# Performance work log

Measured on AMD Instinct MI355X. Metric: run time of the kernel, lower is better.

Reference implementation:

```python
import jax, jax.numpy as jnp
import numpy as np

# Llama-2-7B-like GQA attention, prefill over packed equal-length sequences
H = 4096      # hidden_size
NH = 32       # num_attention_heads
NKV = 8       # num_key_value_heads
HD = H // NH  # head_dim = 128
B = 4         # number of packed sequences
S = 1024      # seq_len per sequence
T = B * S     # total packed tokens
BASE = 10000.0  # rope_theta


def setup_inputs() -> dict:
    key = jax.random.key(0)
    ks = jax.random.split(key, 5)
    x = jax.random.normal(ks[0], (T, H), jnp.float32)
    positions = jnp.tile(jnp.arange(S, dtype=jnp.int32), B)  # per-seq positions
    kv_cache = jnp.zeros((1,), jnp.float32)  # placeholder (prefill: kv from current tokens)
    init = 0.02
    wq = jax.random.normal(ks[1], (NH * HD, H), jnp.float32) * init
    wk = jax.random.normal(ks[2], (NKV * HD, H), jnp.float32) * init
    wv = jax.random.normal(ks[3], (NKV * HD, H), jnp.float32) * init
    wo = jax.random.normal(ks[4], (H, NH * HD), jnp.float32) * init
    return {"x": x, "positions": positions, "kv_cache": kv_cache,
            "wq": wq, "wk": wk, "wv": wv, "wo": wo, "seq_len": S}


def _rope(xh, cos_b, sin_b):
    # xh: [T, Hh, D]; cos_b/sin_b: [T, 1, D] (freqs repeat-interleaved by 2)
    half = xh.shape[-1] // 2
    x_rot = jnp.concatenate([-xh[..., half:], xh[..., :half]], axis=-1)
    return xh * cos_b + x_rot * sin_b


def reference(x, positions, kv_cache, wq, wk, wv, wo, seq_len):
    Tn = x.shape[0]
    q = (x @ wq.T).reshape(Tn, NH, HD)
    k = (x @ wk.T).reshape(Tn, NKV, HD)
    v = (x @ wv.T).reshape(Tn, NKV, HD)
    # GQA: repeat_interleave kv heads
    rep = NH // NKV
    k = jnp.repeat(k, rep, axis=1)
    v = jnp.repeat(v, rep, axis=1)
    # RoPE tables (faithful to _precompute_freqs/_rotary_embeddings)
    inv_freq = 1.0 / (BASE ** (jnp.arange(0, HD, 2, dtype=jnp.float32) / HD))
    t = jnp.arange(seq_len, dtype=jnp.float32)
    freqs = t[:, None] * inv_freq[None, :]            # [S, D/2]
    cos, sin = jnp.cos(freqs), jnp.sin(freqs)
    pos = jnp.clip(positions.astype(jnp.int32), 0, seq_len - 1)
    cos_b = jnp.repeat(cos[pos], 2, axis=-1)[:, None, :]  # [T,1,D]
    sin_b = jnp.repeat(sin[pos], 2, axis=-1)[:, None, :]
    q = _rope(q, cos_b, sin_b)
    k = _rope(k, cos_b, sin_b)
    # Paged attention (prefill): causal attention within each packed sequence
    Bn = Tn // seq_len
    qb = q.reshape(Bn, seq_len, NH, HD)
    kb = k.reshape(Bn, seq_len, NH, HD)
    vb = v.reshape(Bn, seq_len, NH, HD)
    scores = jnp.einsum('bqhd,bkhd->bhqk', qb, kb) * (HD ** -0.5)
    causal = jnp.tril(jnp.ones((seq_len, seq_len), bool))
    scores = jnp.where(causal[None, None], scores, -jnp.inf)
    probs = jax.nn.softmax(scores, axis=-1)
    out = jnp.einsum('bhqk,bkhd->bqhd', probs, vb).reshape(Tn, NH * HD)
    return out @ wo.T
```

## Files before the change

### kernel.cpp

```cpp
#include <hip/hip_runtime.h>
#include <hip/hip_bf16.h>
#include <math.h>

#define T_TOK 4096
#define HID   4096
#define NHQ   32
#define NKVH  8
#define HDIM  128
#define SEQ   1024
#define NBATCH 4

typedef __attribute__((ext_vector_type(8))) short bf16x8;
typedef __attribute__((ext_vector_type(4))) float f32x4;

__device__ __forceinline__ unsigned short f2bf(float f) {
  union { float f; unsigned int u; } x; x.f = f;
  unsigned int r = x.u + 0x7FFFu + ((x.u >> 16) & 1u);
  return (unsigned short)(r >> 16);
}

#define GLOAD_LDS16(gp, lp)                                                        \
  __builtin_amdgcn_global_load_lds(                                                \
      (__attribute__((address_space(1))) void*)(unsigned long long)(const void*)(gp), \
      (__attribute__((address_space(3))) void*)(unsigned long long)(const void*)(lp), \
      16, 0, 0)

__global__ __launch_bounds__(256) void cast_all_k(const float* __restrict__ x,
                                                  const float* __restrict__ wq,
                                                  const float* __restrict__ wk,
                                                  const float* __restrict__ wv,
                                                  const float* __restrict__ wo,
                                                  unsigned short* __restrict__ xb,
                                                  unsigned short* __restrict__ wqkv,
                                                  unsigned short* __restrict__ wob) {
  int i = blockIdx.x * 256 + threadIdx.x;
  const float* src; unsigned short* dst; int off;
  if (i < 4194304)       { src = x;  dst = xb;   off = i; }
  else if (i < 8388608)  { src = wq; dst = wqkv; off = i - 4194304; }
  else if (i < 9437184)  { src = wk; dst = wqkv + 16777216; off = i - 8388608; }
  else if (i < 10485760) { src = wv; dst = wqkv + 20971520; off = i - 9437184; }
  else                   { src = wo; dst = wob;  off = i - 10485760; }
  float4 f = ((const float4*)src)[off];
  ushort4 o;
  o.x = f2bf(f.x); o.y = f2bf(f.y); o.z = f2bf(f.z); o.w = f2bf(f.w);
  ((ushort4*)dst)[off] = o;
}

__global__ __launch_bounds__(512, 2) void gemm_qkv(const unsigned short* __restrict__ A,
                                                   const unsigned short* __restrict__ B,
                                                   const int* __restrict__ pos,
                                                   unsigned short* __restrict__ qr,
                                                   unsigned short* __restrict__ kr,
                                                   unsigned short* __restrict__ vbuf) {
  const int K = 4096, nt = 64;
  __shared__ unsigned short AS[3][16384];
  __shared__ unsigned short BS[3][8192];
  const int tid  = threadIdx.x;
  const int lane = tid & 63;
  const int wave = tid >> 6;
  const int m16  = lane & 15;
  const int quad = lane >> 4;
  const int wm   = wave >> 1;
  const int wn   = wave & 1;

  const int gx = 48;
  const int orig = blockIdx.y * gx + blockIdx.x;
  const int swz = (orig & 7) * 96 + (orig >> 3);
  const long rowBase = (long)(swz / gx) * 256;
  const long colBase = (long)(swz % gx) * 128;

  int aoff[2], boff[2];
#pragma unroll
  for (int ks = 0; ks < 2; ++ks) {
    int sx = ((ks * 4 + quad) ^ (m16 & 7)) * 8;
    aoff[ks] = (wm * 64 + m16) * 64 + sx;
    boff[ks] = (wn * 32 + m16) * 64 + sx;
  }

  const long Kl = K;
  const int sck = ((tid & 7) ^ ((tid >> 3) & 7)) * 8;
  const unsigned short* gA = A + (rowBase + (tid >> 3)) * Kl + sck;
  const unsigned short* gB = B + (colBase + (tid >> 3)) * Kl + sck;
  const int dofs = wave * 512;

#define STG_B(slot_, ko_) { GLOAD_LDS16(gB + (ko_),            &BS[slot_][dofs]);         \
                            GLOAD_LDS16(gB + (ko_) + 64 * Kl,  &BS[slot_][4096 + dofs]); }
#define STG_A(slot_, ko_) { GLOAD_LDS16(gA + (ko_),            &AS[slot_][dofs]);         \
                            GLOAD_LDS16(gA + (ko_) + 64 * Kl,  &AS[slot_][4096 + dofs]);  \
                            GLOAD_LDS16(gA + (ko_) + 128 * Kl, &AS[slot_][8192 + dofs]);  \
                            GLOAD_LDS16(gA + (ko_) + 192 * Kl, &AS[slot_][12288 + dofs]); }

  f32x4 acc[4][4] = {};

  STG_A(0, 0); STG_B(0, 0);
  STG_A(1, 64); STG_B(1, 64);
  asm volatile("s_waitcnt vmcnt(6)" ::: "memory");
  __builtin_amdgcn_s_barrier();

  for (int g = 0; g < 22; ++g) {
#pragma unroll
    for (int u = 0; u < 3; ++u) {
      const int t = g * 3 + u;
      if (t < nt) {
        const bool doStage = (t + 2) < nt;
        const long kn = (long)(t + 2) * 64;
        bf16x8 af[4][2], bfr[4][2];
#pragma unroll
        for (int mf = 0; mf < 4; ++mf)
          af[mf][0] = *(const bf16x8*)(&AS[u][aoff[0] + mf * 1024]);
#pragma unroll
        for (int nf = 0; nf < 4; ++nf)
          bfr[nf][0] = *(const bf16x8*)(&BS[u][boff[0] + (nf & 1) * 1024 + (nf >> 1) * 4096]);
        if (doStage) { STG_A((u + 2) % 3, kn); STG_B((u + 2) % 3, kn); }
#pragma unroll
        for (int mf = 0; mf < 4; ++mf)
          af[mf][1] = *(const bf16x8*)(&AS[u][aoff[1] + mf * 1024]);
#pragma unroll
        for (int nf = 0; nf < 4; ++nf)
          bfr[nf][1] = *(const bf16x8*)(&BS[u][boff[1] + (nf & 1) * 1024 + (nf >> 1) * 4096]);
        __builtin_amdgcn_s_setprio(1);
#pragma unroll
        for (int mf = 0; mf < 4; ++mf)
#pragma unroll
          for (int nf = 0; nf < 4; ++nf)
            acc[mf][nf] = __builtin_amdgcn_mfma_f32_16x16x32_bf16(af[mf][0], bfr[nf][0], acc[mf][nf], 0, 0, 0);
#pragma unroll
        for (int mf = 0; mf < 4; ++mf)
#pragma unroll
          for (int nf = 0; nf < 4; ++nf)
            acc[mf][nf] = __builtin_amdgcn_mfma_f32_16x16x32_bf16(af[mf][1], bfr[nf][1], acc[mf][nf], 0, 0, 0);
        __builtin_amdgcn_s_setprio(0);
        if (doStage)        asm volatile("s_waitcnt vmcnt(6)" ::: "memory");
        else if (t + 1 < nt) asm volatile("s_waitcnt vmcnt(0)" ::: "memory");
        __builtin_amdgcn_s_barrier();
      }
    }
  }

  const int n0 = (int)colBase;
  unsigned short* dst;
  int rstride, colofs;
  bool dorope;
  if (n0 < 4096)       { dst = qr;   rstride = NHQ * HDIM;  colofs = n0;        dorope = true; }
  else if (n0 < 5120)  { dst = kr;   rstride = NKVH * HDIM; colofs = n0 - 4096; dorope = true; }
  else                 { dst = vbuf; rstride = NKVH * HDIM; colofs = n0 - 5120; dorope = false; }
  const float c0 = -13.287712379549449f / 64.0f;
  float fA[2], fB[2];
#pragma unroll
  for (int e = 0; e < 2; ++e) {
    int d = wn * 32 + e * 16 + m16;
    fA[e] = exp2f(c0 * (float)(d >> 1));
    fB[e] = exp2f(c0 * (float)((d >> 1) + 32));
  }
#pragma unroll
  for (int mf = 0; mf < 4; ++mf) {
#pragma unroll
    for (int reg = 0; reg < 4; ++reg) {
      int grow = (int)rowBase + wm * 64 + mf * 16 + quad * 4 + reg;
      unsigned short* drow = dst + (long)grow * rstride + colofs;
      if (dorope) {
        int p = pos[grow];
        p = p < 0 ? 0 : (p > SEQ - 1 ? SEQ - 1 : p);
        float pf = (float)p;
#pragma unroll
        for (int e = 0; e < 2; ++e) {
          int d = wn * 32 + e * 16 + m16;
          float lo = acc[mf][e][reg], hi = acc[mf][e + 2][reg];
          float s1, cc1, s2, cc2;
          __sincosf(pf * fA[e], &s1, &cc1);
          __sincosf(pf * fB[e], &s2, &cc2);
          drow[d]      = f2bf(lo * cc1 - hi * s1);
          drow[d + 64] = f2bf(hi * cc2 + lo * s2);
        }
      } else {
#pragma unroll
        for (int e = 0; e < 2; ++e) {
          int d = wn * 32 + e * 16 + m16;
          drow[d]      = f2bf(acc[mf][e][reg]);
          drow[d + 64] = f2bf(acc[mf][e + 2][reg]);
        }
      }
    }
  }
}

__global__ __launch_bounds__(512, 2) void gemm_o(const unsigned short* __restrict__ A,
                                                 const unsigned short* __restrict__ B,
                                                 float* __restrict__ C) {
  const int K = 4096, N = 4096, nt = 128;
  __shared__ unsigned short AS[3][8192];
  __shared__ unsigned short BS[3][8192];
  const int tid  = threadIdx.x;
  const int lane = tid & 63;
  const int wave = tid >> 6;
  const int m16  = lane & 15;
  const int quad = lane >> 4;
  const int wm   = wave >> 2;
  const int wn   = wave & 3;

  const int gx = 16;
  const int orig = blockIdx.y * gx + blockIdx.x;
  const int swz = (orig & 7) * 32 + (orig >> 3);
  const long rowBase = (long)(swz / gx) * 256;
  const long colBase = (long)(swz % gx) * 256;

  const int slot8 = ((quad + 4 * (m16 & 1)) ^ (m16 >> 1)) * 8;
  const int aob = (wm * 64 + (m16 >> 1)) * 64 + slot8;
  const int bob = (wn * 32 + (m16 >> 1)) * 64 + slot8;

  const long Kl = K;
  const int z = (tid & 7) ^ ((tid >> 3) & 7);
  const long srow = 2 * (tid >> 3) + (z >> 2);
  const int sk = (z & 3) * 8;
  const unsigned short* oA = A + (rowBase + srow) * Kl + sk;
  const unsigned short* oB = B + (colBase + srow) * Kl + sk;
  const int dofs = wave * 512;

#define OSTG_A(sl_, ko_) { GLOAD_LDS16(oA + (ko_),            &AS[sl_][dofs]);         \
                           GLOAD_LDS16(oA + (ko_) + 128 * Kl, &AS[sl_][4096 + dofs]); }
#define OSTG_B(sl_, ko_) { GLOAD_LDS16(oB + (ko_),            &BS[sl_][dofs]);         \
                           GLOAD_LDS16(oB + (ko_) + 128 * Kl, &BS[sl_][4096 + dofs]); }

  f32x4 acc[8][4] = {};

  OSTG_A(0, 0);  OSTG_B(0, 0);
  OSTG_A(1, 32); OSTG_B(1, 32);
  asm volatile("s_waitcnt vmcnt(4)" ::: "memory");
  __builtin_amdgcn_s_barrier();

  for (int g = 0; g < 43; ++g) {
#pragma unroll
    for (int u = 0; u < 3; ++u) {
      const int t = g * 3 + u;
      if (t < nt) {
        const bool doStage = (t + 2) < nt;
        const long kn = (long)(t + 2) * 32;
        bf16x8 af[8], bfr[4];
#pragma unroll
        for (int nf = 0; nf < 4; ++nf)
          bfr[nf] = *(const bf16x8*)(&BS[u][bob + nf * 512]);
#pragma unroll
        for (int mf = 0; mf < 4; ++mf)
          af[mf] = *(const bf16x8*)(&AS[u][aob + mf * 512]);
        if (doStage) { OSTG_A((u + 2) % 3, kn); OSTG_B((u + 2) % 3, kn); }
#pragma unroll
        for (int mf = 4; mf < 8; ++mf)
          af[mf] = *(const bf16x8*)(&AS[u][aob + mf * 512]);
        __builtin_amdgcn_s_setprio(1);
#pragma unroll
        for (int mf = 0; mf < 4; ++mf)
#pragma unroll
          for (int nf = 0; nf < 4; ++nf)
            acc[mf][nf] = __builtin_amdgcn_mfma_f32_16x16x32_bf16(af[mf], bfr[nf], acc[mf][nf], 0, 0, 0);
#pragma unroll
        for (int mf = 4; mf < 8; ++mf)
#pragma unroll
          for (int nf = 0; nf < 4; ++nf)
            acc[mf][nf] = __builtin_amdgcn_mfma_f32_16x16x32_bf16(af[mf], bfr[nf], acc[mf][nf], 0, 0, 0);
        __builtin_amdgcn_s_setprio(0);
        if (doStage)         asm volatile("s_waitcnt vmcnt(4)" ::: "memory");
        else if (t + 1 < nt) asm volatile("s_waitcnt vmcnt(0)" ::: "memory");
        __builtin_amdgcn_s_barrier();
      }
    }
  }

#pragma unroll
  for (int mf = 0; mf < 8; ++mf)
#pragma unroll
    for (int nf = 0; nf < 4; ++nf) {
      long c = colBase + wn * 64 + nf * 16 + m16;
#pragma unroll
      for (int reg = 0; reg < 4; ++reg) {
        long row = rowBase + wm * 128 + mf * 16 + quad * 4 + reg;
        C[row * N + c] = acc[mf][nf][reg];
      }
    }
}

#define ATT_SCALE_L2 0.12754227022f
__global__ __launch_bounds__(256) void attn_k(const unsigned short* __restrict__ Qp,
                                              const unsigned short* __restrict__ Kp,
                                              const unsigned short* __restrict__ Vp,
                                              unsigned short* __restrict__ Op) {
  const int pr = blockIdx.x, h = blockIdx.y, b = blockIdx.z;
  const int kvh = h >> 2;
  const int tid = threadIdx.x, wave = tid >> 6, lane = tid & 63;
  const int m16 = lane & 15, quad = lane >> 4;

  __shared__ unsigned short Ks[2][64][128];
  __shared__ unsigned short Vt[2][128][64];
  __shared__ unsigned short Ps[4][32][64];

  const unsigned short* Kh = Kp + (long)(b * SEQ) * (NKVH * HDIM) + kvh * HDIM;
  const unsigned short* Vh = Vp + (long)(b * SEQ) * (NKVH * HDIM) + kvh * HDIM;

#define STAGE_K(ktv, bufp) {                                               \
    _Pragma("unroll")                                                      \
    for (int it_ = 0; it_ < 4; ++it_) {                                    \
      int c_ = it_ * 256 + tid;                                            \
      int row_ = c_ >> 4, psg_ = c_ & 15;                                  \
      int sg_ = (psg_ & 8) | ((psg_ & 7) ^ (row_ & 7));                    \
      GLOAD_LDS16(Kh + ((long)(ktv) * 64 + row_) * (NKVH * HDIM) + sg_ * 8,\
                  ((unsigned short*)(bufp)) + (it_ * 256 + wave * 64) * 8);\
    } }

#define LOAD_V(ktv, dvv) {                                                 \
    _Pragma("unroll")                                                      \
    for (int it_ = 0; it_ < 4; ++it_)                                      \
      dvv[it_] = *(const uint4*)(Vh + ((long)(ktv) * 64 + lane) * (NKVH * HDIM) + (it_ * 4 + wave) * 8); }

#define SCATTER_V(bufp, dvv) {                                             \
    _Pragma("unroll")                                                      \
    for (int it_ = 0; it_ < 4; ++it_) {                                    \
      const unsigned short* pv_ = (const unsigned short*)&dvv[it_];        \
      int seg_ = it_ * 4 + wave;                                           \
      _Pragma("unroll")                                                    \
      for (int e_ = 0; e_ < 8; ++e_) {                                     \
        int d_ = seg_ * 8 + e_;                                            \
        (bufp)[d_][((((lane >> 3) + d_) & 7) * 8) + (lane & 7)] = pv_[e_]; \
      } } }

  for (int pass = 0; pass < 2; ++pass) {
    const int qt = pass ? pr : (7 - pr);
    const int qbase = qt * 128;
    const int wq_lo = qbase + wave * 32;

    bf16x8 qa[2][4];
#pragma unroll
    for (int i = 0; i < 2; ++i) {
      const unsigned short* qrow =
          Qp + (long)(b * SEQ + wq_lo + i * 16 + m16) * (NHQ * HDIM) + h * HDIM;
#pragma unroll
      for (int kk = 0; kk < 4; ++kk)
        qa[i][kk] = *(const bf16x8*)(qrow + kk * 32 + quad * 8);
    }

    f32x4 o[2][8] = {};
    float mrow[2][4], lrow[2][4];
#pragma unroll
    for (int i = 0; i < 2; ++i)
#pragma unroll
      for (int r = 0; r < 4; ++r) { mrow[i][r] = -1e30f; lrow[i][r] = 0.f; }

    const int nkt = qt * 2 + 2;

    {
      STAGE_K(0, Ks[0]);
      uint4 dv[4];
      LOAD_V(0, dv);
      asm volatile("s_waitcnt vmcnt(0)" ::: "memory");
      SCATTER_V(Vt[0], dv);
    }
    __syncthreads();

    for (int kt = 0; kt < nkt; ++kt) {
      const int cb = kt & 1;
      const bool active = (kt * 64) <= (wq_lo + 31);
      const bool more = (kt + 1) < nkt;

      f32x4 s4[2][4] = {};
      if (active) {
        __builtin_amdgcn_s_setprio(1);
#pragma unroll
        for (int kk = 0; kk < 4; ++kk) {
          bf16x8 kbf[4];
#pragma unroll
          for (int j = 0; j < 4; ++j) {
            int row = j * 16 + m16;
            int cl = kk * 4 + quad;
            int ps = (cl & 8) | ((cl & 7) ^ (row & 7));
            kbf[j] = *(const bf16x8*)(&Ks[cb][row][ps * 8]);
          }
#pragma unroll
          for (int i = 0; i < 2; ++i)
#pragma unroll
            for (int j = 0; j < 4; ++j)
              s4[i][j] = __builtin_amdgcn_mfma_f32_16x16x32_bf16(qa[i][kk], kbf[j], s4[i][j], 0, 0, 0);
        }
        __builtin_amdgcn_s_setprio(0);
      }

      uint4 dv[4];
      if (more) {
        STAGE_K(kt + 1, Ks[cb ^ 1]);
        LOAD_V(kt + 1, dv);
      }
      asm volatile("" ::: "memory");

      if (active) {
        const bool full = (kt * 64 + 63) <= wq_lo;
#pragma unroll
        for (int i = 0; i < 2; ++i) {
#pragma unroll
          for (int r = 0; r < 4; ++r) {
            const int qrow = i * 16 + quad * 4 + r;
            const int qi = qbase + wave * 32 + qrow;
            float v[4];
#pragma unroll
            for (int j = 0; j < 4; ++j) {
              v[j] = s4[i][j][r] * ATT_SCALE_L2;
              if (!full && (kt * 64 + j * 16 + m16 > qi)) v[j] = -1e30f;
            }
            float mx = fmaxf(fmaxf(v[0], v[1]), fmaxf(v[2], v[3]));
            mx = fmaxf(mx, __shfl_xor(mx, 1));
            mx = fmaxf(mx, __shfl_xor(mx, 2));
            mx = fmaxf(mx, __shfl_xor(mx, 4));
            mx = fmaxf(mx, __shfl_xor(mx, 8));
            float mold = mrow[i][r];
            float mnew = fmaxf(mold, mx);
            float alpha = exp2f(mold - mnew);
            float rs = 0.f;
#pragma unroll
            for (int j = 0; j < 4; ++j) {
              float pj = exp2f(v[j] - mnew);
              rs += pj;
              int col = j * 16 + m16;
              Ps[wave][qrow][((((col >> 3) + qrow) & 7) * 8) + (col & 7)] = f2bf(pj);
            }
            rs += __shfl_xor(rs, 1); rs += __shfl_xor(rs, 2);
            rs += __shfl_xor(rs, 4); rs += __shfl_xor(rs, 8);
            lrow[i][r] = lrow[i][r] * alpha + rs;
            mrow[i][r] = mnew;
#pragma unroll
            for (int n = 0; n < 8; ++n) o[i][n][r] *= alpha;
          }
        }
        __builtin_amdgcn_s_setprio(1);
#pragma unroll
        for (int kk = 0; kk < 2; ++kk) {
          bf16x8 pa[2], vb[8];
#pragma unroll
          for (int i = 0; i < 2; ++i) {
            int row = i * 16 + m16;
            pa[i] = *(const bf16x8*)(&Ps[wave][row][(((kk * 4 + quad) + row) & 7) * 8]);
          }
#pragma unroll
          for (int n = 0; n < 8; ++n) {
            int row = n * 16 + m16;
            vb[n] = *(const bf16x8*)(&Vt[cb][row][(((kk * 4 + quad) + row) & 7) * 8]);
          }
#pragma unroll
          for (int i = 0; i < 2; ++i)
#pragma unroll
            for (int n = 0; n < 8; ++n)
              o[i][n] = __builtin_amdgcn_mfma_f32_16x16x32_bf16(pa[i], vb[n], o[i][n], 0, 0, 0);
        }
        __builtin_amdgcn_s_setprio(0);
      }

      if (more) {
        asm volatile("s_waitcnt vmcnt(0)" ::: "memory");
        SCATTER_V(Vt[cb ^ 1], dv);
      }
      __syncthreads();
    }

#pragma unroll
    for (int i = 0; i < 2; ++i) {
#pragma unroll
      for (int r = 0; r < 4; ++r) {
        float inv = 1.0f / lrow[i][r];
        unsigned short* orow =
            Op + (long)(b * SEQ + wq_lo + i * 16 + quad * 4 + r) * (NHQ * HDIM) + h * HDIM;
#pragma unroll
        for (int n = 0; n < 8; ++n)
          orow[n * 16 + m16] = f2bf(o[i][n][r] * inv);
      }
    }
  }
}

extern "C" void kernel_launch(void* const* d_in, const int* in_sizes, int n_in,
                              void* d_out, int out_size, void* d_ws, size_t ws_size,
                              hipStream_t stream) {
  (void)in_sizes; (void)n_in; (void)out_size; (void)ws_size;
  const float* x  = (const float*)d_in[0];
  const int* pos  = (const int*)d_in[1];
  const float* wq = (const float*)d_in[3];
  const float* wk = (const float*)d_in[4];
  const float* wv = (const float*)d_in[5];
  const float* wo = (const float*)d_in[6];
  float* out = (float*)d_out;

  char* ws = (char*)d_ws;
  unsigned short* xb    = (unsigned short*)(ws);
  unsigned short* wqkv  = (unsigned short*)(ws + (32ll << 20));
  unsigned short* wob   = (unsigned short*)(ws + (80ll << 20));
  unsigned short* qr    = (unsigned short*)(ws + (112ll << 20));
  unsigned short* kr    = (unsigned short*)(ws + (144ll << 20));
  unsigned short* vb_   = (unsigned short*)(ws + (152ll << 20));
  unsigned short* ao    = (unsigned short*)(ws + (160ll << 20));

  cast_all_k<<<57344, 256, 0, stream>>>(x, wq, wk, wv, wo, xb, wqkv, wob);
  gemm_qkv<<<dim3(48, 16), 512, 0, stream>>>(xb, wqkv, pos, qr, kr, vb_);
  attn_k<<<dim3(4, 32, 4), 256, 0, stream>>>(qr, kr, vb_, ao);
  gemm_o<<<dim3(16, 16), 512, 0, stream>>>(ao, wob, out);
}
```

Baseline: 744.4 us.

## Split GEMM k-step into two barrier-synchronized half phases to interleave loads and MFMA

Both the QKV-projection GEMM and the output-projection GEMM inner loops are restructured into two sub-phases per k-tile. Each phase loads a half set of fragments from LDS, issues part of the next-tile global-to-LDS staging (A in one phase, B in the other), then synchronizes with a barrier and waits on LDS counters before running that half's MFMAs. This is a ping-pong style schedule meant to keep waves in lockstep, halve fragment register pressure, and spread global loads across the step. It adds two extra barriers per iteration, which may cost time if the waves were already overlapping well.

```diff
diff --git a/kernel.cpp b/kernel.cpp
--- a/kernel.cpp
+++ b/kernel.cpp
@@ -104,33 +104,43 @@
       if (t < nt) {
         const bool doStage = (t + 2) < nt;
         const long kn = (long)(t + 2) * 64;
-        bf16x8 af[4][2], bfr[4][2];
-#pragma unroll
-        for (int mf = 0; mf < 4; ++mf)
-          af[mf][0] = *(const bf16x8*)(&AS[u][aoff[0] + mf * 1024]);
+        bf16x8 af[4], bfr[4];
+
+#pragma unroll
+        for (int mf = 0; mf < 4; ++mf)
+          af[mf] = *(const bf16x8*)(&AS[u][aoff[0] + mf * 1024]);
 #pragma unroll
         for (int nf = 0; nf < 4; ++nf)
-          bfr[nf][0] = *(const bf16x8*)(&BS[u][boff[0] + (nf & 1) * 1024 + (nf >> 1) * 4096]);
-        if (doStage) { STG_A((u + 2) % 3, kn); STG_B((u + 2) % 3, kn); }
-#pragma unroll
-        for (int mf = 0; mf < 4; ++mf)
-          af[mf][1] = *(const bf16x8*)(&AS[u][aoff[1] + mf * 1024]);
+          bfr[nf] = *(const bf16x8*)(&BS[u][boff[0] + (nf & 1) * 1024 + (nf >> 1) * 4096]);
+        if (doStage) STG_A((u + 2) % 3, kn);
+        __builtin_amdgcn_s_barrier();
+        asm volatile("s_waitcnt lgkmcnt(0)" ::: "memory");
+        __builtin_amdgcn_s_setprio(1);
+#pragma unroll
+        for (int mf = 0; mf < 4; ++mf)
+#pragma unroll
+          for (int nf = 0; nf < 4; ++nf)
+            acc[mf][nf] = __builtin_amdgcn_mfma_f32_16x16x32_bf16(af[mf], bfr[nf], acc[mf][nf], 0, 0, 0);
+        __builtin_amdgcn_s_setprio(0);
+        __builtin_amdgcn_s_barrier();
+
+#pragma unroll
+        for (int mf = 0; mf < 4; ++mf)
+          af[mf] = *(const bf16x8*)(&AS[u][aoff[1] + mf * 1024]);
 #pragma unroll
         for (int nf = 0; nf < 4; ++nf)
-          bfr[nf][1] = *(const bf16x8*)(&BS[u][boff[1] + (nf & 1) * 1024 + (nf >> 1) * 4096]);
+          bfr[nf] = *(const bf16x8*)(&BS[u][boff[1] + (nf & 1) * 1024 + (nf >> 1) * 4096]);
+        if (doStage) STG_B((u + 2) % 3, kn);
+        __builtin_amdgcn_s_barrier();
+        asm volatile("s_waitcnt lgkmcnt(0)" ::: "memory");
         __builtin_amdgcn_s_setprio(1);
 #pragma unroll
         for (int mf = 0; mf < 4; ++mf)
 #pragma unroll
           for (int nf = 0; nf < 4; ++nf)
-            acc[mf][nf] = __builtin_amdgcn_mfma_f32_16x16x32_bf16(af[mf][0], bfr[nf][0], acc[mf][nf], 0, 0, 0);
-#pragma unroll
-        for (int mf = 0; mf < 4; ++mf)
-#pragma unroll
-          for (int nf = 0; nf < 4; ++nf)
-            acc[mf][nf] = __builtin_amdgcn_mfma_f32_16x16x32_bf16(af[mf][1], bfr[nf][1], acc[mf][nf], 0, 0, 0);
+            acc[mf][nf] = __builtin_amdgcn_mfma_f32_16x16x32_bf16(af[mf], bfr[nf], acc[mf][nf], 0, 0, 0);
         __builtin_amdgcn_s_setprio(0);
-        if (doStage)        asm volatile("s_waitcnt vmcnt(6)" ::: "memory");
+        if (doStage)         asm volatile("s_waitcnt vmcnt(6)" ::: "memory");
         else if (t + 1 < nt) asm volatile("s_waitcnt vmcnt(0)" ::: "memory");
         __builtin_amdgcn_s_barrier();
       }
@@ -235,28 +245,38 @@
       if (t < nt) {
         const bool doStage = (t + 2) < nt;
         const long kn = (long)(t + 2) * 32;
-        bf16x8 af[8], bfr[4];
+        bf16x8 af[4], bfr[4];
+
 #pragma unroll
         for (int nf = 0; nf < 4; ++nf)
           bfr[nf] = *(const bf16x8*)(&BS[u][bob + nf * 512]);
 #pragma unroll
         for (int mf = 0; mf < 4; ++mf)
           af[mf] = *(const bf16x8*)(&AS[u][aob + mf * 512]);
-        if (doStage) { OSTG_A((u + 2) % 3, kn); OSTG_B((u + 2) % 3, kn); }
-#pragma unroll
-        for (int mf = 4; mf < 8; ++mf)
-          af[mf] = *(const bf16x8*)(&AS[u][aob + mf * 512]);
+        if (doStage) OSTG_A((u + 2) % 3, kn);
+        __builtin_amdgcn_s_barrier();
+        asm volatile("s_waitcnt lgkmcnt(0)" ::: "memory");
         __builtin_amdgcn_s_setprio(1);
 #pragma unroll
         for (int mf = 0; mf < 4; ++mf)
 #pragma unroll
           for (int nf = 0; nf < 4; ++nf)
             acc[mf][nf] = __builtin_amdgcn_mfma_f32_16x16x32_bf16(af[mf], bfr[nf], acc[mf][nf], 0, 0, 0);
-#pragma unroll
-        for (int mf = 4; mf < 8; ++mf)
+        __builtin_amdgcn_s_setprio(0);
+        __builtin_amdgcn_s_barrier();
+
+#pragma unroll
+        for (int mf = 0; mf < 4; ++mf)
+          af[mf] = *(const bf16x8*)(&AS[u][aob + (4 + mf) * 512]);
+        if (doStage) OSTG_B((u + 2) % 3, kn);
+        __builtin_amdgcn_s_barrier();
+        asm volatile("s_waitcnt lgkmcnt(0)" ::: "memory");
+        __builtin_amdgcn_s_setprio(1);
+#pragma unroll
+        for (int mf = 0; mf < 4; ++mf)
 #pragma unroll
           for (int nf = 0; nf < 4; ++nf)
-            acc[mf][nf] = __builtin_amdgcn_mfma_f32_16x16x32_bf16(af[mf], bfr[nf], acc[mf][nf], 0, 0, 0);
+            acc[4 + mf][nf] = __builtin_amdgcn_mfma_f32_16x16x32_bf16(af[mf], bfr[nf], acc[4 + mf][nf], 0, 0, 0);
         __builtin_amdgcn_s_setprio(0);
         if (doStage)         asm volatile("s_waitcnt vmcnt(4)" ::: "memory");
         else if (t + 1 < nt) asm volatile("s_waitcnt vmcnt(0)" ::: "memory");
```

New measurement: 750.0 us. About the same (+0.8%).

## Unify QKV and output GEMMs into one 256x256-tile kernel with 4-stage pipeline

Applied to the files above, without the earlier changes.

Replaces the separate QKV GEMM (256x128 tiles, 3-stage) and output GEMM with a single templated 256x256-tile kernel. It uses a 4-slot LDS ring that prefetches three tiles ahead and reads the next tile's fragments from LDS right after the MFMAs, with the RoPE epilogue fused in for the QKV variant. The wave-to-column mapping changes so each wave's accumulator columns line up with RoPE head pairs. The attention kernel drops V double buffering in favour of a single Vt buffer plus an extra barrier. The aim is more data reuse and better load/compute overlap, at the cost of one block per CU (launch_bounds 512,1), fewer QKV blocks (384) and an added sync in attention.

```diff
diff --git a/kernel.cpp b/kernel.cpp
--- a/kernel.cpp
+++ b/kernel.cpp
@@ -46,150 +46,18 @@
   ((ushort4*)dst)[off] = o;
 }
 
-__global__ __launch_bounds__(512, 2) void gemm_qkv(const unsigned short* __restrict__ A,
-                                                   const unsigned short* __restrict__ B,
-                                                   const int* __restrict__ pos,
-                                                   unsigned short* __restrict__ qr,
-                                                   unsigned short* __restrict__ kr,
-                                                   unsigned short* __restrict__ vbuf) {
-  const int K = 4096, nt = 64;
-  __shared__ unsigned short AS[3][16384];
-  __shared__ unsigned short BS[3][8192];
-  const int tid  = threadIdx.x;
-  const int lane = tid & 63;
-  const int wave = tid >> 6;
-  const int m16  = lane & 15;
-  const int quad = lane >> 4;
-  const int wm   = wave >> 1;
-  const int wn   = wave & 1;
-
-  const int gx = 48;
-  const int orig = blockIdx.y * gx + blockIdx.x;
-  const int swz = (orig & 7) * 96 + (orig >> 3);
-  const long rowBase = (long)(swz / gx) * 256;
-  const long colBase = (long)(swz % gx) * 128;
-
-  int aoff[2], boff[2];
-#pragma unroll
-  for (int ks = 0; ks < 2; ++ks) {
-    int sx = ((ks * 4 + quad) ^ (m16 & 7)) * 8;
-    aoff[ks] = (wm * 64 + m16) * 64 + sx;
-    boff[ks] = (wn * 32 + m16) * 64 + sx;
-  }
-
-  const long Kl = K;
-  const int sck = ((tid & 7) ^ ((tid >> 3) & 7)) * 8;
-  const unsigned short* gA = A + (rowBase + (tid >> 3)) * Kl + sck;
-  const unsigned short* gB = B + (colBase + (tid >> 3)) * Kl + sck;
-  const int dofs = wave * 512;
-
-#define STG_B(slot_, ko_) { GLOAD_LDS16(gB + (ko_),            &BS[slot_][dofs]);         \
-                            GLOAD_LDS16(gB + (ko_) + 64 * Kl,  &BS[slot_][4096 + dofs]); }
-#define STG_A(slot_, ko_) { GLOAD_LDS16(gA + (ko_),            &AS[slot_][dofs]);         \
-                            GLOAD_LDS16(gA + (ko_) + 64 * Kl,  &AS[slot_][4096 + dofs]);  \
-                            GLOAD_LDS16(gA + (ko_) + 128 * Kl, &AS[slot_][8192 + dofs]);  \
-                            GLOAD_LDS16(gA + (ko_) + 192 * Kl, &AS[slot_][12288 + dofs]); }
-
-  f32x4 acc[4][4] = {};
-
-  STG_A(0, 0); STG_B(0, 0);
-  STG_A(1, 64); STG_B(1, 64);
-  asm volatile("s_waitcnt vmcnt(6)" ::: "memory");
-  __builtin_amdgcn_s_barrier();
-
-  for (int g = 0; g < 22; ++g) {
-#pragma unroll
-    for (int u = 0; u < 3; ++u) {
-      const int t = g * 3 + u;
-      if (t < nt) {
-        const bool doStage = (t + 2) < nt;
-        const long kn = (long)(t + 2) * 64;
-        bf16x8 af[4][2], bfr[4][2];
-#pragma unroll
-        for (int mf = 0; mf < 4; ++mf)
-          af[mf][0] = *(const bf16x8*)(&AS[u][aoff[0] + mf * 1024]);
-#pragma unroll
-        for (int nf = 0; nf < 4; ++nf)
-          bfr[nf][0] = *(const bf16x8*)(&BS[u][boff[0] + (nf & 1) * 1024 + (nf >> 1) * 4096]);
-        if (doStage) { STG_A((u + 2) % 3, kn); STG_B((u + 2) % 3, kn); }
-#pragma unroll
-        for (int mf = 0; mf < 4; ++mf)
-          af[mf][1] = *(const bf16x8*)(&AS[u][aoff[1] + mf * 1024]);
-#pragma unroll
-        for (int nf = 0; nf < 4; ++nf)
-          bfr[nf][1] = *(const bf16x8*)(&BS[u][boff[1] + (nf & 1) * 1024 + (nf >> 1) * 4096]);
-        __builtin_amdgcn_s_setprio(1);
-#pragma unroll
-        for (int mf = 0; mf < 4; ++mf)
-#pragma unroll
-          for (int nf = 0; nf < 4; ++nf)
-            acc[mf][nf] = __builtin_amdgcn_mfma_f32_16x16x32_bf16(af[mf][0], bfr[nf][0], acc[mf][nf], 0, 0, 0);
-#pragma unroll
-        for (int mf = 0; mf < 4; ++mf)
-#pragma unroll
-          for (int nf = 0; nf < 4; ++nf)
-            acc[mf][nf] = __builtin_amdgcn_mfma_f32_16x16x32_bf16(af[mf][1], bfr[nf][1], acc[mf][nf], 0, 0, 0);
-        __builtin_amdgcn_s_setprio(0);
-        if (doStage)        asm volatile("s_waitcnt vmcnt(6)" ::: "memory");
-        else if (t + 1 < nt) asm volatile("s_waitcnt vmcnt(0)" ::: "memory");
-        __builtin_amdgcn_s_barrier();
-      }
-    }
-  }
-
-  const int n0 = (int)colBase;
-  unsigned short* dst;
-  int rstride, colofs;
-  bool dorope;
-  if (n0 < 4096)       { dst = qr;   rstride = NHQ * HDIM;  colofs = n0;        dorope = true; }
-  else if (n0 < 5120)  { dst = kr;   rstride = NKVH * HDIM; colofs = n0 - 4096; dorope = true; }
-  else                 { dst = vbuf; rstride = NKVH * HDIM; colofs = n0 - 5120; dorope = false; }
-  const float c0 = -13.287712379549449f / 64.0f;
-  float fA[2], fB[2];
-#pragma unroll
-  for (int e = 0; e < 2; ++e) {
-    int d = wn * 32 + e * 16 + m16;
-    fA[e] = exp2f(c0 * (float)(d >> 1));
-    fB[e] = exp2f(c0 * (float)((d >> 1) + 32));
-  }
-#pragma unroll
-  for (int mf = 0; mf < 4; ++mf) {
-#pragma unroll
-    for (int reg = 0; reg < 4; ++reg) {
-      int grow = (int)rowBase + wm * 64 + mf * 16 + quad * 4 + reg;
-      unsigned short* drow = dst + (long)grow * rstride + colofs;
-      if (dorope) {
-        int p = pos[grow];
-        p = p < 0 ? 0 : (p > SEQ - 1 ? SEQ - 1 : p);
-        float pf = (float)p;
-#pragma unroll
-        for (int e = 0; e < 2; ++e) {
-          int d = wn * 32 + e * 16 + m16;
-          float lo = acc[mf][e][reg], hi = acc[mf][e + 2][reg];
-          float s1, cc1, s2, cc2;
-          __sincosf(pf * fA[e], &s1, &cc1);
-          __sincosf(pf * fB[e], &s2, &cc2);
-          drow[d]      = f2bf(lo * cc1 - hi * s1);
-          drow[d + 64] = f2bf(hi * cc2 + lo * s2);
-        }
-      } else {
-#pragma unroll
-        for (int e = 0; e < 2; ++e) {
-          int d = wn * 32 + e * 16 + m16;
-          drow[d]      = f2bf(acc[mf][e][reg]);
-          drow[d + 64] = f2bf(acc[mf][e + 2][reg]);
-        }
-      }
-    }
-  }
-}
-
-__global__ __launch_bounds__(512, 2) void gemm_o(const unsigned short* __restrict__ A,
-                                                 const unsigned short* __restrict__ B,
-                                                 float* __restrict__ C) {
-  const int K = 4096, N = 4096, nt = 128;
-  __shared__ unsigned short AS[3][8192];
-  __shared__ unsigned short BS[3][8192];
+template<bool FUSED>
+__global__ __launch_bounds__(512, 1) void gemm256(const unsigned short* __restrict__ A,
+                                                  const unsigned short* __restrict__ B,
+                                                  float* __restrict__ C,
+                                                  const int* __restrict__ pos,
+                                                  unsigned short* __restrict__ qr,
+                                                  unsigned short* __restrict__ kr,
+                                                  unsigned short* __restrict__ vbuf,
+                                                  int N) {
+  const int K = 4096, nt = 128;
+  __shared__ unsigned short AS[4][8192];
+  __shared__ unsigned short BS[4][8192];
   const int tid  = threadIdx.x;
   const int lane = tid & 63;
   const int wave = tid >> 6;
@@ -197,85 +65,131 @@
   const int quad = lane >> 4;
   const int wm   = wave >> 2;
   const int wn   = wave & 3;
-
-  const int gx = 16;
+  const int hh   = wn >> 1;
+  const int bb   = (wn & 1) * 32;
+
+  const int gx = gridDim.x;
+  const int nwg = gx * gridDim.y;
   const int orig = blockIdx.y * gx + blockIdx.x;
-  const int swz = (orig & 7) * 32 + (orig >> 3);
+  const int swz = (orig & 7) * (nwg >> 3) + (orig >> 3);
   const long rowBase = (long)(swz / gx) * 256;
   const long colBase = (long)(swz % gx) * 256;
 
   const int slot8 = ((quad + 4 * (m16 & 1)) ^ (m16 >> 1)) * 8;
   const int aob = (wm * 64 + (m16 >> 1)) * 64 + slot8;
-  const int bob = (wn * 32 + (m16 >> 1)) * 64 + slot8;
+  const int bob = (hh * 64 + (wn & 1) * 16 + (m16 >> 1)) * 64 + slot8;
 
   const long Kl = K;
   const int z = (tid & 7) ^ ((tid >> 3) & 7);
   const long srow = 2 * (tid >> 3) + (z >> 2);
   const int sk = (z & 3) * 8;
-  const unsigned short* oA = A + (rowBase + srow) * Kl + sk;
-  const unsigned short* oB = B + (colBase + srow) * Kl + sk;
+  const unsigned short* sA = A + (rowBase + srow) * Kl + sk;
+  const unsigned short* sB = B + (colBase + srow) * Kl + sk;
   const int dofs = wave * 512;
 
-#define OSTG_A(sl_, ko_) { GLOAD_LDS16(oA + (ko_),            &AS[sl_][dofs]);         \
-                           GLOAD_LDS16(oA + (ko_) + 128 * Kl, &AS[sl_][4096 + dofs]); }
-#define OSTG_B(sl_, ko_) { GLOAD_LDS16(oB + (ko_),            &BS[sl_][dofs]);         \
-                           GLOAD_LDS16(oB + (ko_) + 128 * Kl, &BS[sl_][4096 + dofs]); }
+#define STG_A(sl_, ko_) { GLOAD_LDS16(sA + (ko_),            &AS[sl_][dofs]);         \
+                          GLOAD_LDS16(sA + (ko_) + 128 * Kl, &AS[sl_][4096 + dofs]); }
+#define STG_B(sl_, ko_) { GLOAD_LDS16(sB + (ko_),            &BS[sl_][dofs]);         \
+                          GLOAD_LDS16(sB + (ko_) + 128 * Kl, &BS[sl_][4096 + dofs]); }
+
+#define RD_TILE(sl_) {                                                               \
+    _Pragma("unroll")                                                                \
+    for (int nf = 0; nf < 4; ++nf)                                                   \
+      bfr[nf] = *(const bf16x8*)(&BS[sl_][bob + (nf & 1) * 512 + (nf >> 1) * 2048]); \
+    _Pragma("unroll")                                                                \
+    for (int mf = 0; mf < 8; ++mf)                                                   \
+      af[mf] = *(const bf16x8*)(&AS[sl_][aob + mf * 512]); }
 
   f32x4 acc[8][4] = {};
-
-  OSTG_A(0, 0);  OSTG_B(0, 0);
-  OSTG_A(1, 32); OSTG_B(1, 32);
+  bf16x8 af[8], bfr[4];
+
+  STG_A(0, 0);  STG_B(0, 0);
+  STG_A(1, 32); STG_B(1, 32);
+  STG_A(2, 64); STG_B(2, 64);
   asm volatile("s_waitcnt vmcnt(4)" ::: "memory");
   __builtin_amdgcn_s_barrier();
-
-  for (int g = 0; g < 43; ++g) {
-#pragma unroll
-    for (int u = 0; u < 3; ++u) {
-      const int t = g * 3 + u;
-      if (t < nt) {
-        const bool doStage = (t + 2) < nt;
-        const long kn = (long)(t + 2) * 32;
-        bf16x8 af[8], bfr[4];
+  RD_TILE(0);
+
+  for (int g = 0; g < 32; ++g) {
+#pragma unroll
+    for (int u = 0; u < 4; ++u) {
+      const int t = g * 4 + u;
+      if (t + 3 < nt) { STG_A((u + 3) & 3, (t + 3) * 32); STG_B((u + 3) & 3, (t + 3) * 32); }
+      if (t + 3 < nt) asm volatile("s_waitcnt vmcnt(4)" ::: "memory");
+      else            asm volatile("s_waitcnt vmcnt(0)" ::: "memory");
+      __builtin_amdgcn_s_setprio(1);
+#pragma unroll
+      for (int mf = 0; mf < 8; ++mf)
 #pragma unroll
         for (int nf = 0; nf < 4; ++nf)
-          bfr[nf] = *(const bf16x8*)(&BS[u][bob + nf * 512]);
-#pragma unroll
-        for (int mf = 0; mf < 4; ++mf)
-          af[mf] = *(const bf16x8*)(&AS[u][aob + mf * 512]);
-        if (doStage) { OSTG_A((u + 2) % 3, kn); OSTG_B((u + 2) % 3, kn); }
-#pragma unroll
-        for (int mf = 4; mf < 8; ++mf)
-          af[mf] = *(const bf16x8*)(&AS[u][aob + mf * 512]);
-        __builtin_amdgcn_s_setprio(1);
-#pragma unroll
-        for (int mf = 0; mf < 4; ++mf)
-#pragma unroll
-          for (int nf = 0; nf < 4; ++nf)
-            acc[mf][nf] = __builtin_amdgcn_mfma_f32_16x16x32_bf16(af[mf], bfr[nf], acc[mf][nf], 0, 0, 0);
-#pragma unroll
-        for (int mf = 4; mf < 8; ++mf)
-#pragma unroll
-          for (int nf = 0; nf < 4; ++nf)
-            acc[mf][nf] = __builtin_amdgcn_mfma_f32_16x16x32_bf16(af[mf], bfr[nf], acc[mf][nf], 0, 0, 0);
-        __builtin_amdgcn_s_setprio(0);
-        if (doStage)         asm volatile("s_waitcnt vmcnt(4)" ::: "memory");
-        else if (t + 1 < nt) asm volatile("s_waitcnt vmcnt(0)" ::: "memory");
-        __builtin_amdgcn_s_barrier();
-      }
+          acc[mf][nf] = __builtin_amdgcn_mfma_f32_16x16x32_bf16(af[mf], bfr[nf], acc[mf][nf], 0, 0, 0);
+      __builtin_amdgcn_s_setprio(0);
+      if (t + 1 < nt) RD_TILE((u + 1) & 3);
+      __builtin_amdgcn_s_barrier();
     }
   }
 
-#pragma unroll
-  for (int mf = 0; mf < 8; ++mf)
-#pragma unroll
-    for (int nf = 0; nf < 4; ++nf) {
-      long c = colBase + wn * 64 + nf * 16 + m16;
-#pragma unroll
-      for (int reg = 0; reg < 4; ++reg) {
-        long row = rowBase + wm * 128 + mf * 16 + quad * 4 + reg;
-        C[row * N + c] = acc[mf][nf][reg];
-      }
-    }
+  if (!FUSED) {
+#pragma unroll
+    for (int mf = 0; mf < 8; ++mf)
+#pragma unroll
+      for (int nf = 0; nf < 4; ++nf) {
+        long c = colBase + hh * 128 + bb + (nf & 1) * 16 + (nf >> 1) * 64 + m16;
+#pragma unroll
+        for (int reg = 0; reg < 4; ++reg) {
+          long row = rowBase + wm * 128 + mf * 16 + quad * 4 + reg;
+          C[row * N + c] = acc[mf][nf][reg];
+        }
+      }
+    return;
+  }
+
+  const int n0 = (int)colBase;
+  unsigned short* dst;
+  int rstride, colofs0;
+  bool dorope;
+  if (n0 < 4096)       { dst = qr;   rstride = NHQ * HDIM;  colofs0 = n0;        dorope = true; }
+  else if (n0 < 5120)  { dst = kr;   rstride = NKVH * HDIM; colofs0 = n0 - 4096; dorope = true; }
+  else                 { dst = vbuf; rstride = NKVH * HDIM; colofs0 = n0 - 5120; dorope = false; }
+  const int colofs = colofs0 + hh * 128;
+  const float c0 = -13.287712379549449f / 64.0f;
+  float fA[2], fB[2];
+#pragma unroll
+  for (int e = 0; e < 2; ++e) {
+    int d = bb + e * 16 + m16;
+    fA[e] = exp2f(c0 * (float)(d >> 1));
+    fB[e] = exp2f(c0 * (float)((d >> 1) + 32));
+  }
+#pragma unroll
+  for (int mf = 0; mf < 8; ++mf) {
+#pragma unroll
+    for (int reg = 0; reg < 4; ++reg) {
+      int grow = (int)rowBase + wm * 128 + mf * 16 + quad * 4 + reg;
+      unsigned short* drow = dst + (long)grow * rstride + colofs;
+      if (dorope) {
+        int p = pos[grow];
+        p = p < 0 ? 0 : (p > SEQ - 1 ? SEQ - 1 : p);
+        float pf = (float)p;
+#pragma unroll
+        for (int e = 0; e < 2; ++e) {
+          int d = bb + e * 16 + m16;
+          float lo = acc[mf][e][reg], hi = acc[mf][e + 2][reg];
+          float s1, cc1, s2, cc2;
+          __sincosf(pf * fA[e], &s1, &cc1);
+          __sincosf(pf * fB[e], &s2, &cc2);
+          drow[d]      = f2bf(lo * cc1 - hi * s1);
+          drow[d + 64] = f2bf(hi * cc2 + lo * s2);
+        }
+      } else {
+#pragma unroll
+        for (int e = 0; e < 2; ++e) {
+          int d = bb + e * 16 + m16;
+          drow[d]      = f2bf(acc[mf][e][reg]);
+          drow[d + 64] = f2bf(acc[mf][e + 2][reg]);
+        }
+      }
+    }
+  }
 }
 
 #define ATT_SCALE_L2 0.12754227022f
@@ -289,7 +203,7 @@
   const int m16 = lane & 15, quad = lane >> 4;
 
   __shared__ unsigned short Ks[2][64][128];
-  __shared__ unsigned short Vt[2][128][64];
+  __shared__ unsigned short Vt[128][64];
   __shared__ unsigned short Ps[4][32][64];
 
   const unsigned short* Kh = Kp + (long)(b * SEQ) * (NKVH * HDIM) + kvh * HDIM;
@@ -310,7 +224,7 @@
     for (int it_ = 0; it_ < 4; ++it_)                                      \
       dvv[it_] = *(const uint4*)(Vh + ((long)(ktv) * 64 + lane) * (NKVH * HDIM) + (it_ * 4 + wave) * 8); }
 
-#define SCATTER_V(bufp, dvv) {                                             \
+#define SCATTER_V(dvv) {                                                   \
     _Pragma("unroll")                                                      \
     for (int it_ = 0; it_ < 4; ++it_) {                                    \
       const unsigned short* pv_ = (const unsigned short*)&dvv[it_];        \
@@ -318,7 +232,7 @@
       _Pragma("unroll")                                                    \
       for (int e_ = 0; e_ < 8; ++e_) {                                     \
         int d_ = seg_ * 8 + e_;                                            \
-        (bufp)[d_][((((lane >> 3) + d_) & 7) * 8) + (lane & 7)] = pv_[e_]; \
+        Vt[d_][((((lane >> 3) + d_) & 7) * 8) + (lane & 7)] = pv_[e_];     \
       } } }
 
   for (int pass = 0; pass < 2; ++pass) {
@@ -347,10 +261,10 @@
 
     {
       STAGE_K(0, Ks[0]);
-      uint4 dv[4];
-      LOAD_V(0, dv);
+      uint4 dv0[4];
+      LOAD_V(0, dv0);
       asm volatile("s_waitcnt vmcnt(0)" ::: "memory");
-      SCATTER_V(Vt[0], dv);
+      SCATTER_V(dv0);
     }
     __syncthreads();
 
@@ -438,7 +352,7 @@
 #pragma unroll
           for (int n = 0; n < 8; ++n) {
             int row = n * 16 + m16;
-            vb[n] = *(const bf16x8*)(&Vt[cb][row][(((kk * 4 + quad) + row) & 7) * 8]);
+            vb[n] = *(const bf16x8*)(&Vt[row][(((kk * 4 + quad) + row) & 7) * 8]);
           }
 #pragma unroll
           for (int i = 0; i < 2; ++i)
@@ -449,10 +363,8 @@
         __builtin_amdgcn_s_setprio(0);
       }
 
-      if (more) {
-        asm volatile("s_waitcnt vmcnt(0)" ::: "memory");
-        SCATTER_V(Vt[cb ^ 1], dv);
-      }
+      __syncthreads();
+      if (more) SCATTER_V(dv);
       __syncthreads();
     }
 
@@ -493,7 +405,7 @@
   unsigned short* ao    = (unsigned short*)(ws + (160ll << 20));
 
   cast_all_k<<<57344, 256, 0, stream>>>(x, wq, wk, wv, wo, xb, wqkv, wob);
-  gemm_qkv<<<dim3(48, 16), 512, 0, stream>>>(xb, wqkv, pos, qr, kr, vb_);
+  gemm256<true><<<dim3(24, 16), 512, 0, stream>>>(xb, wqkv, nullptr, pos, qr, kr, vb_, 6144);
   attn_k<<<dim3(4, 32, 4), 256, 0, stream>>>(qr, kr, vb_, ao);
-  gemm_o<<<dim3(16, 16), 512, 0, stream>>>(ao, wob, out);
+  gemm256<false><<<dim3(16, 16), 512, 0, stream>>>(ao, wob, out, nullptr, nullptr, nullptr, nullptr, 4096);
 }
```

Measured after the change: 754.6 us. No clear change (+1.4%).
